# Kernel optimization log

Hardware: AMD Instinct MI355X
Metric: run time of the kernel (lower is better)

Reference implementation:

```python
import jax, jax.numpy as jnp
import numpy as np

N_NODES = 50000
N_EDGES = 800000
IN_DIM, HID_DIM, EMB_DIM = 128, 256, 64


def setup_inputs() -> dict:
    key = jax.random.key(0)
    ks = jax.random.split(key, 10)
    x = jax.random.normal(ks[0], (N_NODES, IN_DIM), dtype=jnp.float32)
    edge_index = jax.random.randint(ks[1], (2, N_EDGES), 0, N_NODES, dtype=jnp.int64)
    def glorot(k, fan_in, fan_out):
        s = jnp.sqrt(6.0 / (fan_in + fan_out))
        return jax.random.uniform(k, (fan_in, fan_out), jnp.float32, -s, s)
    return {
        "x": x,
        "edge_index": edge_index,
        "W1": glorot(ks[2], IN_DIM, HID_DIM), "b1": jnp.zeros((HID_DIM,), jnp.float32),
        "W2": glorot(ks[3], HID_DIM, EMB_DIM), "b2": jnp.zeros((EMB_DIM,), jnp.float32),
        "W3": glorot(ks[4], EMB_DIM, HID_DIM), "b3": jnp.zeros((HID_DIM,), jnp.float32),
        "W4": glorot(ks[5], HID_DIM, IN_DIM), "b4": jnp.zeros((IN_DIM,), jnp.float32),
    }


def _gcn_conv(x, W, b, src, dst, norm, n_nodes):
    # linear transform, then edge gather -> normalize -> scatter-add (PyG GCNConv)
    h = x @ W                                    # [N, out]
    msg = h[src] * norm[:, None]                 # [E+N, out]
    out = jax.ops.segment_sum(msg, dst, num_segments=n_nodes)
    return out + b


def reference(x, edge_index, W1, b1, W2, b2, W3, b3, W4, b4):
    n = x.shape[0]
    loops = jnp.arange(n, dtype=edge_index.dtype)
    src = jnp.concatenate([edge_index[0], loops])  # add self-loops
    dst = jnp.concatenate([edge_index[1], loops])
    # symmetric degree normalization: deg computed on destination incl. self-loops
    deg = jax.ops.segment_sum(jnp.ones_like(dst, dtype=x.dtype), dst, num_segments=n)
    dis = jax.lax.rsqrt(jnp.maximum(deg, 1.0))
    norm = dis[src] * dis[dst]                   # [E+N]

    h = jax.nn.relu(_gcn_conv(x, W1, b1, src, dst, norm, n))
    h = jax.nn.relu(_gcn_conv(h, W2, b2, src, dst, norm, n))
    h = jax.nn.relu(_gcn_conv(h, W3, b3, src, dst, norm, n))
    out = _gcn_conv(h, W4, b4, src, dst, norm, n)
    return out
```

## Files before the change

kernel.cpp:

```cpp
#include <hip/hip_runtime.h>

#define N_NODES 50000
#define N_EDGES 800000

static inline size_t align256(size_t x) { return (x + 255) & ~(size_t)255; }

typedef _Float16 f16x8 __attribute__((ext_vector_type(8)));
typedef float f32x4 __attribute__((ext_vector_type(4)));
typedef float f32x8 __attribute__((ext_vector_type(8)));


__global__ void count_kernel(const int* __restrict__ dst, int* __restrict__ counts,
                             int* __restrict__ rank, int E) {
    int e = blockIdx.x * blockDim.x + threadIdx.x;
    if (e < E) rank[e] = atomicAdd(&counts[dst[e]], 1);
}

__global__ void scan1_kernel(const int* __restrict__ counts, int* __restrict__ row_ptr,
                             int* __restrict__ bsum, int n) {
    __shared__ int sd[1024];
    int i = blockIdx.x * 1024 + threadIdx.x;
    int v = (i < n) ? counts[i] : 0;
    sd[threadIdx.x] = v;
    __syncthreads();
    #pragma unroll
    for (int off = 1; off < 1024; off <<= 1) {
        int t = 0;
        if ((int)threadIdx.x >= off) t = sd[threadIdx.x - off];
        __syncthreads();
        sd[threadIdx.x] += t;
        __syncthreads();
    }
    if (i < n) row_ptr[i + 1] = sd[threadIdx.x];
    if (threadIdx.x == 1023) bsum[blockIdx.x] = sd[1023];
}

__global__ void scan3_kernel(int* __restrict__ row_ptr, const int* __restrict__ bsum,
                             const int* __restrict__ counts, float* __restrict__ dis, int n) {
    __shared__ int pfx_s;
    if (threadIdx.x == 0) {
        int nb = blockIdx.x >> 2;
        int p = 0;
        for (int j = 0; j < nb; ++j) p += bsum[j];
        pfx_s = p;
    }
    __syncthreads();
    int i = blockIdx.x * blockDim.x + threadIdx.x;
    if (i < n) {
        row_ptr[i + 1] += pfx_s;
        dis[i] = rsqrtf((float)(counts[i] + 1));
        if (i == 0) row_ptr[0] = 0;
    }
}

__global__ void fill_kernel(const int* __restrict__ src, const int* __restrict__ dst,
                            const int* __restrict__ rank, const int* __restrict__ row_ptr,
                            int* __restrict__ col, int E) {
    int e = blockIdx.x * blockDim.x + threadIdx.x;
    if (e < E) col[row_ptr[dst[e]] + rank[e]] = src[e];
}


__device__ __forceinline__ void pack_dev(const float* __restrict__ W,
                                         _Float16* __restrict__ Ph, _Float16* __restrict__ Pl,
                                         int K, int N, int id) {
    int l = id & 63;
    int f = id >> 6;
    int nf16 = N >> 4;
    int ks = f / nf16, nf = f - ks * nf16;
    int k0 = ks * 32 + (l >> 4) * 8;
    int n  = nf * 16 + (l & 15);
    #pragma unroll
    for (int j = 0; j < 8; ++j) {
        float v = W[(size_t)(k0 + j) * N + n];
        _Float16 hi = (_Float16)v;
        Ph[(size_t)id * 8 + j] = hi;
        Pl[(size_t)id * 8 + j] = (_Float16)(v - (float)hi);
    }
}

__global__ void prep_kernel(const float* __restrict__ W1, _Float16* __restrict__ w1h, _Float16* __restrict__ w1l,
                            const float* __restrict__ W2, _Float16* __restrict__ w2h, _Float16* __restrict__ w2l,
                            const float* __restrict__ W3, _Float16* __restrict__ w3h, _Float16* __restrict__ w3l,
                            const float* __restrict__ W4, _Float16* __restrict__ w4h, _Float16* __restrict__ w4l,
                            const float* __restrict__ x, const float* __restrict__ dis,
                            _Float16* __restrict__ xs) {
    int b = blockIdx.x;
    int tid = threadIdx.x;
    if (b < 16) {
        pack_dev(W1, w1h, w1l, 128, 256, b * 256 + tid);
    } else if (b < 24) {
        pack_dev(W2, w2h, w2l, 256, 64, (b - 16) * 256 + tid);
    } else if (b < 32) {
        pack_dev(W3, w3h, w3l, 64, 256, (b - 24) * 256 + tid);
    } else if (b < 48) {
        pack_dev(W4, w4h, w4l, 256, 128, (b - 32) * 256 + tid);
    } else {
        int q = (b - 48) * 256 + tid;
        if (q < N_NODES * 16) {
            int v = q >> 4, o = q & 15;
            float s = dis[v];
            const float* px = x + (size_t)v * 128 + o * 8;
            float4 t0 = *(const float4*)px;
            float4 t1 = *(const float4*)(px + 4);
            f16x8 h;
            h[0] = (_Float16)(s * t0.x); h[1] = (_Float16)(s * t0.y);
            h[2] = (_Float16)(s * t0.z); h[3] = (_Float16)(s * t0.w);
            h[4] = (_Float16)(s * t1.x); h[5] = (_Float16)(s * t1.y);
            h[6] = (_Float16)(s * t1.z); h[7] = (_Float16)(s * t1.w);
            ((f16x8*)xs)[q] = h;
        }
    }
}


template <int K1, int N2>
__global__ __launch_bounds__(256) void fused_pair(
    const _Float16* __restrict__ gin, const int* __restrict__ row_ptr,
    const int* __restrict__ colx, const float* __restrict__ dis,
    const float* __restrict__ bias1,
    const _Float16* __restrict__ B1h, const _Float16* __restrict__ B1l,
    const _Float16* __restrict__ B2h, const _Float16* __restrict__ B2l,
    _Float16* __restrict__ G16, int M) {

    constexpr int KS  = K1 / 32;
    constexpr int OPR = K1 / 8;
    constexpr int NF2 = N2 / 16;
    constexpr int NT2 = N2 / 64;
    constexpr int CS  = 16 / NF2;
    constexpr int KT2 = 8 / CS;

    __shared__ __align__(16) char ldsb[69632];
    f16x8* stg = (f16x8*)ldsb;

    const int t = threadIdx.x, w = t >> 6, l = t & 63;
    const int lrow = l & 15, lh = l >> 4;
    const int m0 = blockIdx.x * 64 + w * 16;
    const int v = m0 + lrow;
    const bool okv = v < M;

    const f16x8* g8 = (const f16x8*)gin;
    f32x8 sums[KS];
    #pragma unroll
    for (int ks = 0; ks < KS; ++ks) sums[ks] = (f32x8){};
    int s = 0, e = 0;
    if (okv) {
        s = row_ptr[v]; e = row_ptr[v + 1];
        #pragma unroll
        for (int ks = 0; ks < KS; ++ks)
            sums[ks] = __builtin_convertvector(g8[(size_t)v * OPR + ks * 4 + lh], f32x8);
    }
    int i = s;
    for (; i + 4 <= e; i += 4) {
        int u0 = colx[i], u1 = colx[i + 1], u2 = colx[i + 2], u3 = colx[i + 3];
        #pragma unroll
        for (int ks = 0; ks < KS; ++ks) {
            f32x8 f0 = __builtin_convertvector(g8[(size_t)u0 * OPR + ks * 4 + lh], f32x8);
            f32x8 f1 = __builtin_convertvector(g8[(size_t)u1 * OPR + ks * 4 + lh], f32x8);
            f32x8 f2 = __builtin_convertvector(g8[(size_t)u2 * OPR + ks * 4 + lh], f32x8);
            f32x8 f3 = __builtin_convertvector(g8[(size_t)u3 * OPR + ks * 4 + lh], f32x8);
            sums[ks] += (f0 + f1) + (f2 + f3);
        }
    }
    for (; i < e; ++i) {
        int u = colx[i];
        #pragma unroll
        for (int ks = 0; ks < KS; ++ks)
            sums[ks] += __builtin_convertvector(g8[(size_t)u * OPR + ks * 4 + lh], f32x8);
    }
    const float dv = okv ? dis[v] : 0.f;
    f16x8 pah[KS], pal[KS];
    #pragma unroll
    for (int ks = 0; ks < KS; ++ks)
        #pragma unroll
        for (int j = 0; j < 8; ++j) {
            float r = dv * sums[ks][j];
            pah[ks][j] = (_Float16)r;
            pal[ks][j] = (_Float16)(r - (float)pah[ks][j]);
        }

    const f16x8* b1h8 = (const f16x8*)B1h;
    const f16x8* b1l8 = (const f16x8*)B1l;
    f16x8 ph[4], pl[4];
    #pragma unroll
    for (int j = 0; j < 4; ++j) { ph[j] = b1h8[j * 256 + t]; pl[j] = b1l8[j * 256 + t]; }

    f32x4 acc1[4][4] = {};
    #pragma unroll
    for (int ks = 0; ks < KS; ++ks) {
        const int cur = ks & 1;
        #pragma unroll
        for (int j = 0; j < 4; ++j) {
            stg[(cur * 2 + 0) * 1024 + j * 256 + t] = ph[j];
            stg[(cur * 2 + 1) * 1024 + j * 256 + t] = pl[j];
        }
        if (ks + 1 < KS) {
            #pragma unroll
            for (int j = 0; j < 4; ++j) {
                ph[j] = b1h8[(size_t)(ks + 1) * 1024 + j * 256 + t];
                pl[j] = b1l8[(size_t)(ks + 1) * 1024 + j * 256 + t];
            }
        }
        __syncthreads();
        const f16x8* lbh = stg + (cur * 2 + 0) * 1024;
        const f16x8* lbl = stg + (cur * 2 + 1) * 1024;
        #pragma unroll
        for (int nt = 0; nt < 4; ++nt)
            #pragma unroll
            for (int c = 0; c < 4; ++c) {
                f16x8 bh = lbh[(nt * 4 + c) * 64 + l];
                f16x8 bl = lbl[(nt * 4 + c) * 64 + l];
                acc1[nt][c] = __builtin_amdgcn_mfma_f32_16x16x32_f16(pah[ks], bh, acc1[nt][c], 0, 0, 0);
                acc1[nt][c] = __builtin_amdgcn_mfma_f32_16x16x32_f16(pal[ks], bh, acc1[nt][c], 0, 0, 0);
                acc1[nt][c] = __builtin_amdgcn_mfma_f32_16x16x32_f16(pah[ks], bl, acc1[nt][c], 0, 0, 0);
            }
    }
    __syncthreads();

    float* xp = (float*)ldsb + (size_t)w * 4352;
    #pragma unroll
    for (int nt = 0; nt < 4; ++nt)
        #pragma unroll
        for (int c = 0; c < 4; ++c) {
            float bb = bias1[nt * 64 + c * 16 + lrow];
            #pragma unroll
            for (int r = 0; r < 4; ++r) {
                float hv = fmaxf(acc1[nt][c][r] + bb, 0.f);
                xp[(nt * 64 + c * 16 + lrow) * 17 + lh * 4 + r] = hv;
            }
        }

    const f16x8* b2h8 = (const f16x8*)B2h;
    const f16x8* b2l8 = (const f16x8*)B2l;
    #pragma unroll
    for (int j = 0; j < 4; ++j) { ph[j] = b2h8[j * 256 + t]; pl[j] = b2l8[j * 256 + t]; }

    f16x8 a2h[8], a2l[8];
    #pragma unroll
    for (int ks2 = 0; ks2 < 8; ++ks2)
        #pragma unroll
        for (int j = 0; j < 8; ++j) {
            float vv = xp[(ks2 * 32 + lh * 8 + j) * 17 + lrow];
            a2h[ks2][j] = (_Float16)vv;
            a2l[ks2][j] = (_Float16)(vv - (float)a2h[ks2][j]);
        }
    __syncthreads();

    f32x4 acc2[NT2][4] = {};
    #pragma unroll
    for (int kc = 0; kc < KT2; ++kc) {
        const int cur = kc & 1;
        #pragma unroll
        for (int j = 0; j < 4; ++j) {
            stg[(cur * 2 + 0) * 1024 + j * 256 + t] = ph[j];
            stg[(cur * 2 + 1) * 1024 + j * 256 + t] = pl[j];
        }
        if (kc + 1 < KT2) {
            #pragma unroll
            for (int j = 0; j < 4; ++j) {
                ph[j] = b2h8[(size_t)(kc + 1) * 1024 + j * 256 + t];
                pl[j] = b2l8[(size_t)(kc + 1) * 1024 + j * 256 + t];
            }
        }
        __syncthreads();
        const f16x8* lbh = stg + (cur * 2 + 0) * 1024;
        const f16x8* lbl = stg + (cur * 2 + 1) * 1024;
        #pragma unroll
        for (int cs = 0; cs < CS; ++cs) {
            const int ks2 = kc * CS + cs;
            #pragma unroll
            for (int nt2 = 0; nt2 < NT2; ++nt2)
                #pragma unroll
                for (int c = 0; c < 4; ++c) {
                    f16x8 bh = lbh[(cs * NF2 + nt2 * 4 + c) * 64 + l];
                    f16x8 bl = lbl[(cs * NF2 + nt2 * 4 + c) * 64 + l];
                    acc2[nt2][c] = __builtin_amdgcn_mfma_f32_16x16x32_f16(a2h[ks2], bh, acc2[nt2][c], 0, 0, 0);
                    acc2[nt2][c] = __builtin_amdgcn_mfma_f32_16x16x32_f16(a2l[ks2], bh, acc2[nt2][c], 0, 0, 0);
                    acc2[nt2][c] = __builtin_amdgcn_mfma_f32_16x16x32_f16(a2h[ks2], bl, acc2[nt2][c], 0, 0, 0);
                }
        }
    }

    #pragma unroll
    for (int nt2 = 0; nt2 < NT2; ++nt2)
        #pragma unroll
        for (int r = 0; r < 4; ++r) {
            int m = m0 + lh * 4 + r;
            if (m < M) {
                float sc = dis[m];
                #pragma unroll
                for (int c = 0; c < 4; ++c)
                    G16[(size_t)m * N2 + nt2 * 64 + c * 16 + lrow] = (_Float16)(sc * acc2[nt2][c][r]);
            }
        }
}


template <int MODE, int DQ8>
__global__ __launch_bounds__(256) void agg8(
    const _Float16* __restrict__ g, const int* __restrict__ row_ptr,
    const int* __restrict__ col, const float* __restrict__ dis,
    const float* __restrict__ bias, float* __restrict__ outf,
    _Float16* __restrict__ o16) {
    const int NPB = 256 / DQ8;
    int t = threadIdx.x;
    int nl = t / DQ8, c = t % DQ8;
    int v = blockIdx.x * NPB + nl;
    if (v >= N_NODES) return;
    const f16x8* g8 = (const f16x8*)g;
    size_t rowo = (size_t)v * DQ8 + c;

    f32x8 sum = __builtin_convertvector(g8[rowo], f32x8);

    int s = row_ptr[v], e = row_ptr[v + 1];
    int i = s;
    for (; i + 4 <= e; i += 4) {
        int u0 = col[i], u1 = col[i + 1], u2 = col[i + 2], u3 = col[i + 3];
        f32x8 f0 = __builtin_convertvector(g8[(size_t)u0 * DQ8 + c], f32x8);
        f32x8 f1 = __builtin_convertvector(g8[(size_t)u1 * DQ8 + c], f32x8);
        f32x8 f2 = __builtin_convertvector(g8[(size_t)u2 * DQ8 + c], f32x8);
        f32x8 f3 = __builtin_convertvector(g8[(size_t)u3 * DQ8 + c], f32x8);
        sum += (f0 + f1) + (f2 + f3);
    }
    for (; i < e; ++i)
        sum += __builtin_convertvector(g8[(size_t)col[i] * DQ8 + c], f32x8);

    float dv = dis[v];
    f32x8 bv = ((const f32x8*)bias)[c];
    if (MODE == 2) {
        f16x8 h;
        #pragma unroll
        for (int j = 0; j < 8; ++j) {
            float r = fmaxf(dv * sum[j] + bv[j], 0.f) * dv;
            h[j] = (_Float16)r;
        }
        ((f16x8*)o16)[rowo] = h;
    } else {
        f32x8 r;
        #pragma unroll
        for (int j = 0; j < 8; ++j) r[j] = dv * sum[j] + bv[j];
        ((f32x8*)outf)[rowo] = r;
    }
}


extern "C" void kernel_launch(void* const* d_in, const int* in_sizes, int n_in,
                              void* d_out, int out_size, void* d_ws, size_t ws_size,
                              hipStream_t stream) {
    const int N = N_NODES, E = N_EDGES;

    const float* x   = (const float*)d_in[0];
    const int*   ei  = (const int*)d_in[1];
    const int*   src = ei;
    const int*   dst = ei + E;
    const float* W1 = (const float*)d_in[2];  const float* b1 = (const float*)d_in[3];
    const float* W2 = (const float*)d_in[4];  const float* b2 = (const float*)d_in[5];
    const float* W3 = (const float*)d_in[6];  const float* b3 = (const float*)d_in[7];
    const float* W4 = (const float*)d_in[8];  const float* b4 = (const float*)d_in[9];
    float* out = (float*)d_out;

    char* w = (char*)d_ws;
    int*   counts  = (int*)w;    w += align256((size_t)N * 4);
    int*   row_ptr = (int*)w;    w += align256((size_t)(N + 1) * 4);
    float* dis     = (float*)w;  w += align256((size_t)N * 4);
    int*   bsum    = (int*)w;    w += align256((size_t)64 * 4);
    int*   rank    = (int*)w;    w += align256((size_t)E * 4);
    int*   col     = (int*)w;    w += align256((size_t)E * 4);
    _Float16* w1h = (_Float16*)w; w += align256(32768 * 2);
    _Float16* w1l = (_Float16*)w; w += align256(32768 * 2);
    _Float16* w2h = (_Float16*)w; w += align256(16384 * 2);
    _Float16* w2l = (_Float16*)w; w += align256(16384 * 2);
    _Float16* w3h = (_Float16*)w; w += align256(16384 * 2);
    _Float16* w3l = (_Float16*)w; w += align256(16384 * 2);
    _Float16* w4h = (_Float16*)w; w += align256(32768 * 2);
    _Float16* w4l = (_Float16*)w; w += align256(32768 * 2);
    _Float16* xs  = (_Float16*)w; w += align256((size_t)N * 128 * 2);
    _Float16* g2  = (_Float16*)w; w += align256((size_t)N * 64 * 2);
    _Float16* h2s = (_Float16*)w; w += align256((size_t)N * 64 * 2);
    _Float16* gg4 = (_Float16*)w; w += align256((size_t)N * 128 * 2);

    const int nb = (N + 1023) / 1024;
    hipMemsetAsync(counts, 0, (size_t)N * 4, stream);
    count_kernel<<<(E + 255) / 256, 256, 0, stream>>>(dst, counts, rank, E);
    scan1_kernel<<<nb, 1024, 0, stream>>>(counts, row_ptr, bsum, N);
    scan3_kernel<<<(N + 255) / 256, 256, 0, stream>>>(row_ptr, bsum, counts, dis, N);
    fill_kernel<<<(E + 255) / 256, 256, 0, stream>>>(src, dst, rank, row_ptr, col, E);

    prep_kernel<<<48 + (N * 16 + 255) / 256, 256, 0, stream>>>(
        W1, w1h, w1l, W2, w2h, w2l, W3, w3h, w3l, W4, w4h, w4l, x, dis, xs);

    const int gx = (N + 63) / 64;

    fused_pair<128, 64><<<gx, 256, 0, stream>>>(xs, row_ptr, col, dis, b1,
                                                w1h, w1l, w2h, w2l, g2, N);
    agg8<2, 8><<<(N + 31) / 32, 256, 0, stream>>>(g2, row_ptr, col, dis, b2, nullptr, h2s);

    fused_pair<64, 128><<<gx, 256, 0, stream>>>(h2s, row_ptr, col, dis, b3,
                                                w3h, w3l, w4h, w4l, gg4, N);
    agg8<3, 16><<<(N + 15) / 16, 256, 0, stream>>>(gg4, row_ptr, col, dis, b4, out, nullptr);
}
```

Baseline: 261.7 us.

## Split neighbor aggregation out of fused GEMM into separate gather kernel

Moves the sparse neighbor aggregation that was inside the fused GEMM pair kernel into a standalone agg8 pass. That pass writes normalized hi/lo fp16 split activations, which a GEMM-only kernel then reads. The aim is to let the irregular gather run with its own thread mapping and occupancy, instead of being limited by the LDS-heavy GEMM kernel. The cost is extra global-memory round trips for the intermediate buffers and two additional kernel launches. It also moves __syncthreads inside the k-loops.

After: 224.4 us. 14.3% less time.

```diff
diff --git a/kernel.cpp b/kernel.cpp
--- a/kernel.cpp
+++ b/kernel.cpp
@@ -115,16 +115,14 @@
 
 
 template <int K1, int N2>
-__global__ __launch_bounds__(256) void fused_pair(
-    const _Float16* __restrict__ gin, const int* __restrict__ row_ptr,
-    const int* __restrict__ colx, const float* __restrict__ dis,
-    const float* __restrict__ bias1,
+__global__ __launch_bounds__(256) void fused_gemm(
+    const _Float16* __restrict__ Ah, const _Float16* __restrict__ Al,
+    const float* __restrict__ dis, const float* __restrict__ bias1,
     const _Float16* __restrict__ B1h, const _Float16* __restrict__ B1l,
     const _Float16* __restrict__ B2h, const _Float16* __restrict__ B2l,
     _Float16* __restrict__ G16, int M) {
 
     constexpr int KS  = K1 / 32;
-    constexpr int OPR = K1 / 8;
     constexpr int NF2 = N2 / 16;
     constexpr int NT2 = N2 / 64;
     constexpr int CS  = 16 / NF2;
@@ -139,45 +137,15 @@
     const int v = m0 + lrow;
     const bool okv = v < M;
 
-    const f16x8* g8 = (const f16x8*)gin;
-    f32x8 sums[KS];
-    #pragma unroll
-    for (int ks = 0; ks < KS; ++ks) sums[ks] = (f32x8){};
-    int s = 0, e = 0;
-    if (okv) {
-        s = row_ptr[v]; e = row_ptr[v + 1];
-        #pragma unroll
-        for (int ks = 0; ks < KS; ++ks)
-            sums[ks] = __builtin_convertvector(g8[(size_t)v * OPR + ks * 4 + lh], f32x8);
-    }
-    int i = s;
-    for (; i + 4 <= e; i += 4) {
-        int u0 = colx[i], u1 = colx[i + 1], u2 = colx[i + 2], u3 = colx[i + 3];
-        #pragma unroll
-        for (int ks = 0; ks < KS; ++ks) {
-            f32x8 f0 = __builtin_convertvector(g8[(size_t)u0 * OPR + ks * 4 + lh], f32x8);
-            f32x8 f1 = __builtin_convertvector(g8[(size_t)u1 * OPR + ks * 4 + lh], f32x8);
-            f32x8 f2 = __builtin_convertvector(g8[(size_t)u2 * OPR + ks * 4 + lh], f32x8);
-            f32x8 f3 = __builtin_convertvector(g8[(size_t)u3 * OPR + ks * 4 + lh], f32x8);
-            sums[ks] += (f0 + f1) + (f2 + f3);
-        }
-    }
-    for (; i < e; ++i) {
-        int u = colx[i];
-        #pragma unroll
-        for (int ks = 0; ks < KS; ++ks)
-            sums[ks] += __builtin_convertvector(g8[(size_t)u * OPR + ks * 4 + lh], f32x8);
-    }
-    const float dv = okv ? dis[v] : 0.f;
+    f16x8 z8 = {0, 0, 0, 0, 0, 0, 0, 0};
+    const f16x8* pAh = (const f16x8*)(Ah + (size_t)v * K1);
+    const f16x8* pAl = (const f16x8*)(Al + (size_t)v * K1);
     f16x8 pah[KS], pal[KS];
     #pragma unroll
-    for (int ks = 0; ks < KS; ++ks)
-        #pragma unroll
-        for (int j = 0; j < 8; ++j) {
-            float r = dv * sums[ks][j];
-            pah[ks][j] = (_Float16)r;
-            pal[ks][j] = (_Float16)(r - (float)pah[ks][j]);
-        }
+    for (int ks = 0; ks < KS; ++ks) {
+        pah[ks] = okv ? pAh[ks * 4 + lh] : z8;
+        pal[ks] = okv ? pAl[ks * 4 + lh] : z8;
+    }
 
     const f16x8* b1h8 = (const f16x8*)B1h;
     const f16x8* b1l8 = (const f16x8*)B1l;
@@ -214,8 +182,8 @@
                 acc1[nt][c] = __builtin_amdgcn_mfma_f32_16x16x32_f16(pal[ks], bh, acc1[nt][c], 0, 0, 0);
                 acc1[nt][c] = __builtin_amdgcn_mfma_f32_16x16x32_f16(pah[ks], bl, acc1[nt][c], 0, 0, 0);
             }
-    }
-    __syncthreads();
+        __syncthreads();
+    }
 
     float* xp = (float*)ldsb + (size_t)w * 4352;
     #pragma unroll
@@ -279,6 +247,7 @@
                     acc2[nt2][c] = __builtin_amdgcn_mfma_f32_16x16x32_f16(a2h[ks2], bl, acc2[nt2][c], 0, 0, 0);
                 }
         }
+        __syncthreads();
     }
 
     #pragma unroll
@@ -301,7 +270,7 @@
     const _Float16* __restrict__ g, const int* __restrict__ row_ptr,
     const int* __restrict__ col, const float* __restrict__ dis,
     const float* __restrict__ bias, float* __restrict__ outf,
-    _Float16* __restrict__ o16) {
+    _Float16* __restrict__ o16, _Float16* __restrict__ oh, _Float16* __restrict__ ol) {
     const int NPB = 256 / DQ8;
     int t = threadIdx.x;
     int nl = t / DQ8, c = t % DQ8;
@@ -326,8 +295,18 @@
         sum += __builtin_convertvector(g8[(size_t)col[i] * DQ8 + c], f32x8);
 
     float dv = dis[v];
-    f32x8 bv = ((const f32x8*)bias)[c];
-    if (MODE == 2) {
+    if (MODE == 0) {
+        f16x8 h, lo;
+        #pragma unroll
+        for (int j = 0; j < 8; ++j) {
+            float r = dv * sum[j];
+            h[j]  = (_Float16)r;
+            lo[j] = (_Float16)(r - (float)h[j]);
+        }
+        ((f16x8*)oh)[rowo] = h;
+        ((f16x8*)ol)[rowo] = lo;
+    } else if (MODE == 2) {
+        f32x8 bv = ((const f32x8*)bias)[c];
         f16x8 h;
         #pragma unroll
         for (int j = 0; j < 8; ++j) {
@@ -336,6 +315,7 @@
         }
         ((f16x8*)o16)[rowo] = h;
     } else {
+        f32x8 bv = ((const f32x8*)bias)[c];
         f32x8 r;
         #pragma unroll
         for (int j = 0; j < 8; ++j) r[j] = dv * sum[j] + bv[j];
@@ -375,8 +355,12 @@
     _Float16* w4h = (_Float16*)w; w += align256(32768 * 2);
     _Float16* w4l = (_Float16*)w; w += align256(32768 * 2);
     _Float16* xs  = (_Float16*)w; w += align256((size_t)N * 128 * 2);
+    _Float16* t1h = (_Float16*)w; w += align256((size_t)N * 128 * 2);
+    _Float16* t1l = (_Float16*)w; w += align256((size_t)N * 128 * 2);
     _Float16* g2  = (_Float16*)w; w += align256((size_t)N * 64 * 2);
     _Float16* h2s = (_Float16*)w; w += align256((size_t)N * 64 * 2);
+    _Float16* t3h = (_Float16*)w; w += align256((size_t)N * 64 * 2);
+    _Float16* t3l = (_Float16*)w; w += align256((size_t)N * 64 * 2);
     _Float16* gg4 = (_Float16*)w; w += align256((size_t)N * 128 * 2);
 
     const int nb = (N + 1023) / 1024;
@@ -391,11 +375,17 @@
 
     const int gx = (N + 63) / 64;
 
-    fused_pair<128, 64><<<gx, 256, 0, stream>>>(xs, row_ptr, col, dis, b1,
+    agg8<0, 16><<<(N + 15) / 16, 256, 0, stream>>>(xs, row_ptr, col, dis, nullptr,
+                                                   nullptr, nullptr, t1h, t1l);
+    fused_gemm<128, 64><<<gx, 256, 0, stream>>>(t1h, t1l, dis, b1,
                                                 w1h, w1l, w2h, w2l, g2, N);
-    agg8<2, 8><<<(N + 31) / 32, 256, 0, stream>>>(g2, row_ptr, col, dis, b2, nullptr, h2s);
-
-    fused_pair<64, 128><<<gx, 256, 0, stream>>>(h2s, row_ptr, col, dis, b3,
+    agg8<2, 8><<<(N + 31) / 32, 256, 0, stream>>>(g2, row_ptr, col, dis, b2,
+                                                  nullptr, h2s, nullptr, nullptr);
+
+    agg8<0, 8><<<(N + 31) / 32, 256, 0, stream>>>(h2s, row_ptr, col, dis, nullptr,
+                                                  nullptr, nullptr, t3h, t3l);
+    fused_gemm<64, 128><<<gx, 256, 0, stream>>>(t3h, t3l, dis, b3,
                                                 w3h, w3l, w4h, w4l, gg4, N);
-    agg8<3, 16><<<(N + 15) / 16, 256, 0, stream>>>(gg4, row_ptr, col, dis, b4, out, nullptr);
-}
+    agg8<3, 16><<<(N + 15) / 16, 256, 0, stream>>>(gg4, row_ptr, col, dis, b4,
+                                                   out, nullptr, nullptr, nullptr);
+}
```
